# Kernel optimization log

Hardware: AMD Instinct MI355X
Metric: run time of the kernel (lower is better)

Reference implementation:

```python
import jax, jax.numpy as jnp
import numpy as np

D_MODEL = 1024
N_HEADS = 16
D_HEAD = D_MODEL // N_HEADS
SEQ_LEN = 4096
BATCH = 1
WINDOW = 256
NUM_RAND = 32
GLOBAL_TOKENS = (0,)


def _bigbird_mask(seq_len: int) -> jnp.ndarray:
    """Additive mask (0 = attend, -inf = blocked): global + sliding window + random.
    Random token selection is deterministic (fixed seed), mirroring torch.manual_seed(42)."""
    rng = np.random.default_rng(42)
    mask = np.full((seq_len, seq_len), -np.inf, dtype=np.float32)
    idx = np.arange(seq_len)
    # sliding window: |i-j| <= WINDOW (end = i + window + 1 in the original)
    band = np.abs(idx[:, None] - idx[None, :]) <= WINDOW
    mask[band] = 0.0
    # global tokens: full row + full column
    for g in GLOBAL_TOKENS:
        mask[g, :] = 0.0
        mask[:, g] = 0.0
    not_global = ~np.isin(idx, np.array(GLOBAL_TOKENS))
    gset = set(GLOBAL_TOKENS)
    for i in range(seq_len):
        if i in gset:
            continue
        cand = idx[(np.abs(idx - i) > WINDOW) & not_global]
        if cand.size >= NUM_RAND:
            sel = rng.choice(cand, size=NUM_RAND, replace=False)
            mask[i, sel] = 0.0
    return jnp.asarray(mask)


def setup_inputs() -> dict:
    key = jax.random.key(0)
    ks = jax.random.split(key, 9)
    s = 1.0 / np.sqrt(D_MODEL)
    x = jax.random.normal(ks[0], (BATCH, SEQ_LEN, D_MODEL), dtype=jnp.float32)
    # torch.nn.Linear weights are [out_features, in_features]
    Wq = jax.random.normal(ks[1], (D_MODEL, D_MODEL), dtype=jnp.float32) * s
    Wk = jax.random.normal(ks[2], (D_MODEL, D_MODEL), dtype=jnp.float32) * s
    Wv = jax.random.normal(ks[3], (D_MODEL, D_MODEL), dtype=jnp.float32) * s
    Wo = jax.random.normal(ks[4], (D_MODEL, D_MODEL), dtype=jnp.float32) * s
    bq = jax.random.normal(ks[5], (D_MODEL,), dtype=jnp.float32) * s
    bk = jax.random.normal(ks[6], (D_MODEL,), dtype=jnp.float32) * s
    bv = jax.random.normal(ks[7], (D_MODEL,), dtype=jnp.float32) * s
    bo = jax.random.normal(ks[8], (D_MODEL,), dtype=jnp.float32) * s
    mask = _bigbird_mask(SEQ_LEN)
    return {"x": x, "Wq": Wq, "bq": bq, "Wk": Wk, "bk": bk,
            "Wv": Wv, "bv": bv, "Wo": Wo, "bo": bo, "mask": mask}


def reference(x, Wq, bq, Wk, bk, Wv, bv, Wo, bo, mask):
    B, S, D = x.shape
    H, dh = N_HEADS, D_HEAD
    scale = dh ** -0.5
    q = (x @ Wq.T + bq).reshape(B, S, H, dh)  # [B,S,H,dh]
    k = (x @ Wk.T + bk).reshape(B, S, H, dh)
    v = (x @ Wv.T + bv).reshape(B, S, H, dh)
    scores = jnp.einsum("bihd,bjhd->bhij", q, k) * scale + mask  # [B,H,S,S]
    attn = jax.nn.softmax(scores, axis=-1)  # dropout is identity in eval mode
    out = jnp.einsum("bhij,bjhd->bihd", attn, v).reshape(B, S, D)
    return out @ Wo.T + bo
```

## Files before the change

kernel.cpp:

```cpp
#include <hip/hip_runtime.h>

typedef __attribute__((ext_vector_type(8))) short short8;
typedef __attribute__((ext_vector_type(4))) short short4v;
typedef __attribute__((ext_vector_type(4))) float f32x4;
typedef __attribute__((ext_vector_type(4))) float float4v;
typedef __attribute__((ext_vector_type(4))) unsigned uint4v;

#define MFMA16(a, b, c) __builtin_amdgcn_mfma_f32_16x16x32_bf16(a, b, c, 0, 0, 0)

static __device__ __forceinline__ short f2bf(float f) {
  union { float f; unsigned u; } a; a.f = f;
  unsigned r = a.u + 0x7fffu + ((a.u >> 16) & 1u);
  return (short)(r >> 16);
}
static __device__ __forceinline__ float bf2f(short s) {
  union { float f; unsigned u; } a; a.u = ((unsigned)(unsigned short)s) << 16;
  return a.f;
}
static __device__ __forceinline__ float u2f(unsigned u) {
  union { float f; unsigned u; } a; a.u = u;
  return a.f;
}

__global__ __launch_bounds__(256) void k_bitmask(const float* __restrict__ mask,
                                                 unsigned long long* __restrict__ bmT) {
  int wid = blockIdx.x * 4 + (threadIdx.x >> 6);
  int lane = threadIdx.x & 63;
  int ct = wid & 63, r = wid >> 6;
  float v = mask[(size_t)r * 4096 + ct * 64 + lane];
  unsigned long long bal = __ballot(v == 0.0f);
  if (lane == 0) bmT[(size_t)ct * 4096 + r] = bal;
}

__global__ __launch_bounds__(256) void k_randidx(const unsigned long long* __restrict__ bmT,
                                                 unsigned short* __restrict__ ridx,
                                                 unsigned* __restrict__ cntR) {
  int r = blockIdx.x * 4 + (threadIdx.x >> 6);
  int lane = threadIdx.x & 63;
  if (r == 0) {
    if (lane < 32) ridx[lane] = 0;
    if (lane == 0) cntR[0] = 0;
    return;
  }
  int rb = r >> 6;
  bool excl = (lane == 0) || (lane >= rb - 4 && lane <= rb + 4);
  unsigned long long w64 = excl ? 0ull : bmT[(size_t)lane * 4096 + r];
  int cnt = __popcll(w64);
  int p = cnt;
#pragma unroll
  for (int off = 1; off < 64; off <<= 1) {
    int t = __shfl_up(p, off);
    if (lane >= off) p += t;
  }
  int base = p - cnt;
  int total = __shfl(p, 63);
  while (w64) {
    int b = __ffsll((unsigned long long)w64) - 1;
    ridx[(size_t)r * 32 + base] = (unsigned short)(lane * 64 + b);
    ++base;
    w64 &= w64 - 1;
  }
  for (int t = total + lane; t < 32; t += 64) ridx[(size_t)r * 32 + t] = 0;
  if (lane == 63) cntR[r] = (unsigned)p;
}

__global__ __launch_bounds__(256) void k_split(const float* __restrict__ src,
                                               short* __restrict__ hi,
                                               short* __restrict__ lo, int n4) {
  int i = blockIdx.x * 256 + threadIdx.x;
  if (i >= n4) return;
  float4v x = ((const float4v*)src)[i];
  short4v h, l;
#pragma unroll
  for (int j = 0; j < 4; ++j) {
    short hh = f2bf(x[j]);
    h[j] = hh;
    l[j] = f2bf(x[j] - bf2f(hh));
  }
  ((short4v*)hi)[i] = h;
  ((short4v*)lo)[i] = l;
}

__global__ __launch_bounds__(256) void k_splitw(const float* __restrict__ wq,
                                                const float* __restrict__ wk,
                                                const float* __restrict__ wv,
                                                const float* __restrict__ wo,
                                                short* __restrict__ hi,
                                                short* __restrict__ lo) {
  int i = blockIdx.x * 256 + threadIdx.x;
  int row = i >> 8, c4 = i & 255;
  const float* src = row < 1024 ? wq + row * 1024
                   : row < 2048 ? wk + (row - 1024) * 1024
                   : row < 3072 ? wv + (row - 2048) * 1024
                                : wo + (row - 3072) * 1024;
  float4v x = ((const float4v*)src)[c4];
  short4v h, l;
#pragma unroll
  for (int j = 0; j < 4; ++j) {
    short hh = f2bf(x[j]);
    h[j] = hh;
    l[j] = f2bf(x[j] - bf2f(hh));
  }
  ((short4v*)hi)[i] = h;
  ((short4v*)lo)[i] = l;
}

template <int SPLIT, int EPI>
__global__ __launch_bounds__(256) void k_gemm(const short* __restrict__ Agh,
                                              const short* __restrict__ Agl,
                                              const short* __restrict__ Bgh,
                                              const short* __restrict__ Bgl,
                                              const float* __restrict__ b0,
                                              const float* __restrict__ b1,
                                              const float* __restrict__ b2,
                                              short* __restrict__ outb,
                                              float* __restrict__ outf) {
  const int K = 1024;
  const int LDT = 72;
  __shared__ short Ah[128 * LDT];
  __shared__ short Bh[128 * LDT];
  __shared__ short Al[SPLIT ? 128 * LDT : 8];
  __shared__ short Bl[SPLIT ? 128 * LDT : 8];
  int tid = threadIdx.x, lane = tid & 63, w = tid >> 6;
  int bm = blockIdx.x * 128, bn = blockIdx.y * 128;
  int wm = (w >> 1) * 64, wn = (w & 1) * 64;
  int arow = lane & 15, ag = lane >> 4;
  int srow = tid >> 3, sc = (tid & 7) * 8;
  f32x4 acc[4][4] = {};

  for (int k0 = 0; k0 < K; k0 += 64) {
    __syncthreads();
#pragma unroll
    for (int p = 0; p < 4; ++p) {
      int r = srow + p * 32;
      *(short8*)&Ah[r * LDT + sc] = *(const short8*)&Agh[(bm + r) * K + k0 + sc];
      *(short8*)&Bh[r * LDT + sc] = *(const short8*)&Bgh[(bn + r) * K + k0 + sc];
      if (SPLIT) {
        *(short8*)&Al[r * LDT + sc] = *(const short8*)&Agl[(bm + r) * K + k0 + sc];
        *(short8*)&Bl[r * LDT + sc] = *(const short8*)&Bgl[(bn + r) * K + k0 + sc];
      }
    }
    __syncthreads();
#pragma unroll
    for (int kk = 0; kk < 64; kk += 32) {
      int ko = kk + ag * 8;
      short8 af[4], bf[4], afl[4], bfl[4];
#pragma unroll
      for (int mi = 0; mi < 4; ++mi)
        af[mi] = *(const short8*)&Ah[(wm + mi * 16 + arow) * LDT + ko];
#pragma unroll
      for (int ni = 0; ni < 4; ++ni)
        bf[ni] = *(const short8*)&Bh[(wn + ni * 16 + arow) * LDT + ko];
      if (SPLIT) {
#pragma unroll
        for (int mi = 0; mi < 4; ++mi)
          afl[mi] = *(const short8*)&Al[(wm + mi * 16 + arow) * LDT + ko];
#pragma unroll
        for (int ni = 0; ni < 4; ++ni)
          bfl[ni] = *(const short8*)&Bl[(wn + ni * 16 + arow) * LDT + ko];
      }
#pragma unroll
      for (int mi = 0; mi < 4; ++mi)
#pragma unroll
        for (int ni = 0; ni < 4; ++ni) {
          acc[mi][ni] = MFMA16(af[mi], bf[ni], acc[mi][ni]);
          if (SPLIT) {
            acc[mi][ni] = MFMA16(af[mi], bfl[ni], acc[mi][ni]);
            acc[mi][ni] = MFMA16(afl[mi], bf[ni], acc[mi][ni]);
          }
        }
    }
  }
#pragma unroll
  for (int mi = 0; mi < 4; ++mi)
#pragma unroll
    for (int ni = 0; ni < 4; ++ni)
#pragma unroll
      for (int r = 0; r < 4; ++r) {
        int row = bm + wm + mi * 16 + ag * 4 + r;
        int col = bn + wn + ni * 16 + arow;
        float v = acc[mi][ni][r];
        if (EPI == 0) {
          int cl = col & 1023;
          const float* bp = col < 1024 ? b0 : col < 2048 ? b1 : b2;
          v += bp[cl];
          int head = cl >> 6, dh = col & 63, pr = col >> 10;
          outb[pr * (16 * 4096 * 64) + (head * 4096 + row) * 64 + dh] = f2bf(v);
        } else {
          v += b0[col];
          outf[row * 1024 + col] = v;
        }
      }
}

#define QS2 0.18033688f

__global__ __launch_bounds__(256) void k_rand(const short* __restrict__ q,
                                              const short* __restrict__ k,
                                              const short* __restrict__ v,
                                              const unsigned short* __restrict__ ridx,
                                              const unsigned* __restrict__ cntR,
                                              float* __restrict__ RO,
                                              float* __restrict__ RL) {
  __shared__ float Pp[4][4][32];
  __shared__ unsigned Pc[4][4][32];
  __shared__ float R0o[4][64];
  __shared__ float R0l[4];
  int tid = threadIdx.x, lane = tid & 63, w = tid >> 6;
  int bid = blockIdx.x;

  if (bid < 4096) {
    int head = bid & 15, rg = bid >> 4;
    int rbase = rg * 16 + w * 4;
    int rw = lane >> 4;
    int cl = lane & 15;
    int row = rbase + rw;
    const short* kh = k + (size_t)head * 4096 * 64;
    const short* vh = v + (size_t)head * 4096 * 64;
    unsigned cnt = cntR[row];
    unsigned col0 = ridx[(size_t)row * 32 + cl];
    unsigned col1 = ridx[(size_t)row * 32 + 16 + cl];
    const uint4v* qp4 = (const uint4v*)(q + ((size_t)head * 4096 + row) * 64);
    const uint4v* k0 = (const uint4v*)(kh + (size_t)col0 * 64);
    const uint4v* k1 = (const uint4v*)(kh + (size_t)col1 * 64);
    float s0 = 0.f, s1 = 0.f;
#pragma unroll
    for (int i = 0; i < 8; ++i) {
      uint4v qv = qp4[i];
      uint4v a = k0[i];
      uint4v b = k1[i];
#pragma unroll
      for (int jj = 0; jj < 4; ++jj) {
        float qlo = u2f(qv[jj] << 16), qhi = u2f(qv[jj] & 0xffff0000u);
        s0 = fmaf(qlo, u2f(a[jj] << 16), s0);
        s0 = fmaf(qhi, u2f(a[jj] & 0xffff0000u), s0);
        s1 = fmaf(qlo, u2f(b[jj] << 16), s1);
        s1 = fmaf(qhi, u2f(b[jj] & 0xffff0000u), s1);
      }
    }
    float p0 = (cl < (int)cnt) ? exp2f(fmaf(s0, QS2, -32.f)) : 0.f;
    float p1 = (cl + 16 < (int)cnt) ? exp2f(fmaf(s1, QS2, -32.f)) : 0.f;
    float ls = p0 + p1;
#pragma unroll
    for (int off = 1; off < 16; off <<= 1) ls += __shfl_xor(ls, off, 16);
    Pp[w][rw][cl] = p0;
    Pp[w][rw][16 + cl] = p1;
    Pc[w][rw][cl] = col0;
    Pc[w][rw][16 + cl] = col1;
    if (cl == 0 && row != 0) RL[(size_t)head * 4096 + row] = ls;
    int h2 = lane >> 5, r2 = (lane >> 3) & 3, ch = lane & 7;
    float o[8] = {};
#pragma unroll
    for (int i = 0; i < 16; ++i) {
      int ci = h2 * 16 + i;
      float pp = Pp[w][r2][ci];
      unsigned cc = Pc[w][r2][ci];
      uint4v vv = *(const uint4v*)(vh + (size_t)cc * 64 + ch * 8);
#pragma unroll
      for (int jj = 0; jj < 4; ++jj) {
        o[2 * jj] = fmaf(pp, u2f(vv[jj] << 16), o[2 * jj]);
        o[2 * jj + 1] = fmaf(pp, u2f(vv[jj] & 0xffff0000u), o[2 * jj + 1]);
      }
    }
#pragma unroll
    for (int jj = 0; jj < 8; ++jj) o[jj] += __shfl_xor(o[jj], 32);
    int row2 = rbase + r2;
    if (h2 == 0 && row2 != 0) {
      float4v a = {o[0], o[1], o[2], o[3]};
      float4v b = {o[4], o[5], o[6], o[7]};
      float* ro = RO + ((size_t)head * 4096 + row2) * 64 + ch * 8;
      *(float4v*)ro = a;
      *(float4v*)(ro + 4) = b;
    }
  } else {
    int head = bid - 4096;
    const short* kh = k + (size_t)head * 4096 * 64;
    const short* vh = v + (size_t)head * 4096 * 64;
    const uint4v* qp4 = (const uint4v*)(q + (size_t)head * 4096 * 64);
    uint4v qv[8];
#pragma unroll
    for (int i = 0; i < 8; ++i) qv[i] = qp4[i];
    float o[8] = {};
    float lacc = 0.f;
    int grp = lane >> 3, ch8 = lane & 7;
    float* Pw = (float*)Pp[w];
    for (int chk = w; chk < 59; chk += 4) {
      int cb = 320 + chk * 64;
      const uint4v* kp4 = (const uint4v*)(kh + (size_t)(cb + lane) * 64);
      float s2 = 0.f;
#pragma unroll
      for (int i = 0; i < 8; ++i) {
        uint4v kv = kp4[i];
#pragma unroll
        for (int jj = 0; jj < 4; ++jj) {
          s2 = fmaf(u2f(qv[i][jj] << 16), u2f(kv[jj] << 16), s2);
          s2 = fmaf(u2f(qv[i][jj] & 0xffff0000u), u2f(kv[jj] & 0xffff0000u), s2);
        }
      }
      float p = exp2f(fmaf(s2, QS2, -32.f));
      lacc += p;
      Pw[lane] = p;
#pragma unroll
      for (int i = 0; i < 8; ++i) {
        float pp = Pw[grp * 8 + i];
        uint4v vv = *(const uint4v*)(vh + (size_t)(cb + grp * 8 + i) * 64 + ch8 * 8);
#pragma unroll
        for (int jj = 0; jj < 4; ++jj) {
          o[2 * jj] = fmaf(pp, u2f(vv[jj] << 16), o[2 * jj]);
          o[2 * jj + 1] = fmaf(pp, u2f(vv[jj] & 0xffff0000u), o[2 * jj + 1]);
        }
      }
    }
#pragma unroll
    for (int off = 8; off < 64; off <<= 1) {
#pragma unroll
      for (int jj = 0; jj < 8; ++jj) o[jj] += __shfl_xor(o[jj], off);
      lacc += __shfl_xor(lacc, off);
    }
    lacc += __shfl_xor(lacc, 1);
    lacc += __shfl_xor(lacc, 2);
    lacc += __shfl_xor(lacc, 4);
    if (grp == 0) {
#pragma unroll
      for (int jj = 0; jj < 8; ++jj) R0o[w][ch8 * 8 + jj] = o[jj];
    }
    if (lane == 0) R0l[w] = lacc;
    __syncthreads();
    if (w == 0) {
      float o4 = R0o[0][lane] + R0o[1][lane] + R0o[2][lane] + R0o[3][lane];
      RO[(size_t)head * 4096 * 64 + lane] = o4;
      if (lane == 0) RL[(size_t)head * 4096] = R0l[0] + R0l[1] + R0l[2] + R0l[3];
    }
  }
}

__global__ __launch_bounds__(256) void k_flash(const short* __restrict__ q,
                                               const short* __restrict__ k,
                                               const short* __restrict__ v,
                                               const unsigned long long* __restrict__ bmT,
                                               const float* __restrict__ RO,
                                               const float* __restrict__ RL,
                                               short* __restrict__ aoh,
                                               short* __restrict__ aol) {
  const int LDT = 88;
  const int LDP = 72;
  __shared__ short Kl[64 * LDT];
  __shared__ short VT[64 * LDT];
  __shared__ short Pl[4 * 16 * LDP];
  __shared__ unsigned long long BM[64];
  int tid = threadIdx.x, lane = tid & 63, w = tid >> 6;
  int head = blockIdx.x & 15, rb = blockIdx.x >> 4;
  int q0 = rb * 64;
  int arow = lane & 15, ag = lane >> 4;
  int srow = tid >> 3, sc = (tid & 7) * 8;

  const short* qh = q + ((size_t)head * 4096 + q0 + w * 16) * 64;
  const short* kh = k + (size_t)head * 4096 * 64;
  const short* vh = v + (size_t)head * 4096 * 64;
  short8 aq0 = *(const short8*)&qh[arow * 64 + ag * 8];
  short8 aq1 = *(const short8*)&qh[arow * 64 + 32 + ag * 8];

  f32x4 accO[4] = {};
  float m[4] = {-1e30f, -1e30f, -1e30f, -1e30f};
  float lsum[4] = {0.f, 0.f, 0.f, 0.f};

  int t_lo = rb - 4; if (t_lo < 0) t_lo = 0;
  int t_hi = rb + 4; if (t_hi > 63) t_hi = 63;
  int extra0 = (t_lo > 0) ? 1 : 0;
  int nt = t_hi - t_lo + 1 + extra0;

  for (int it = 0; it < nt; ++it) {
    int ct = (extra0 && it == 0) ? 0 : t_lo + it - extra0;
    __syncthreads();
#pragma unroll
    for (int p = 0; p < 2; ++p) {
      int r = srow + p * 32;
      *(short8*)&Kl[r * LDT + sc] = *(const short8*)&kh[(ct * 64 + r) * 64 + sc];
    }
#pragma unroll
    for (int p = 0; p < 2; ++p) {
      int r = srow + p * 32;
      short8 vv = *(const short8*)&vh[(ct * 64 + r) * 64 + sc];
#pragma unroll
      for (int i = 0; i < 8; ++i) {
        int row = sc + i;
        VT[row * LDT + (r ^ (((row >> 3) & 7) << 3))] = vv[i];
      }
    }
    if (tid < 128)
      ((unsigned*)BM)[tid] = ((const unsigned*)(bmT + (size_t)ct * 4096 + q0))[tid];
    __syncthreads();

    f32x4 s[4];
    __builtin_amdgcn_s_setprio(1);
#pragma unroll
    for (int ni = 0; ni < 4; ++ni) {
      short8 b0 = *(const short8*)&Kl[(ni * 16 + arow) * LDT + ag * 8];
      short8 b1 = *(const short8*)&Kl[(ni * 16 + arow) * LDT + 32 + ag * 8];
      f32x4 z = {};
      z = MFMA16(aq0, b0, z);
      z = MFMA16(aq1, b1, z);
      s[ni] = z;
    }
    __builtin_amdgcn_s_setprio(0);
    float pv[4][4], mx[4];
#pragma unroll
    for (int r = 0; r < 4; ++r) {
      unsigned long long wrd = BM[w * 16 + ag * 4 + r];
      unsigned wlo = (unsigned)wrd, whi = (unsigned)(wrd >> 32);
      float rm = -1e30f;
#pragma unroll
      for (int ni = 0; ni < 4; ++ni) {
        unsigned word = (ni < 2) ? wlo : whi;
        unsigned bit = (word >> (arow + (ni & 1) * 16)) & 1u;
        float sv = s[ni][r] * QS2;
        sv = bit ? sv : -1e30f;
        pv[ni][r] = sv;
        rm = fmaxf(rm, sv);
      }
      mx[r] = rm;
    }
#pragma unroll
    for (int off = 1; off < 16; off <<= 1)
#pragma unroll
      for (int r = 0; r < 4; ++r) mx[r] = fmaxf(mx[r], __shfl_xor(mx[r], off, 16));
#pragma unroll
    for (int r = 0; r < 4; ++r) {
      float mnew = fmaxf(m[r], mx[r]);
      float alpha = exp2f(m[r] - mnew);
      m[r] = mnew;
      lsum[r] *= alpha;
      accO[0][r] *= alpha; accO[1][r] *= alpha;
      accO[2][r] *= alpha; accO[3][r] *= alpha;
      float rs = 0.f;
#pragma unroll
      for (int ni = 0; ni < 4; ++ni) {
        float p = exp2f(pv[ni][r] - mnew);
        pv[ni][r] = p;
        rs += p;
      }
#pragma unroll
      for (int off = 1; off < 16; off <<= 1) rs += __shfl_xor(rs, off, 16);
      lsum[r] += rs;
    }
    short* Pw = &Pl[w * 16 * LDP];
#pragma unroll
    for (int r = 0; r < 4; ++r)
#pragma unroll
      for (int ni = 0; ni < 4; ++ni)
        Pw[(ag * 4 + r) * LDP + ni * 16 + arow] = f2bf(pv[ni][r]);
    __builtin_amdgcn_s_setprio(1);
#pragma unroll
    for (int kk2 = 0; kk2 < 2; ++kk2) {
      short8 pa = *(const short8*)&Pw[arow * LDP + kk2 * 32 + ag * 8];
#pragma unroll
      for (int f = 0; f < 4; ++f) {
        int drow = f * 16 + arow;
        int jo = (kk2 * 32 + ag * 8) ^ (((drow >> 3) & 7) << 3);
        short8 vb = *(const short8*)&VT[drow * LDT + jo];
        accO[f] = MFMA16(pa, vb, accO[f]);
      }
    }
    __builtin_amdgcn_s_setprio(0);
  }

#pragma unroll
  for (int r = 0; r < 4; ++r) {
    int rr = ag * 4 + r;
    int row = q0 + w * 16 + rr;
    float mF = fmaxf(m[r], 32.0f);
    float ab = exp2f(m[r] - mF);
    float aR = exp2f(32.0f - mF);
    float lR = RL[(size_t)head * 4096 + row];
    float lt = lsum[r] * ab + lR * aR;
#pragma unroll
    for (int f = 0; f < 4; ++f) {
      float o = accO[f][r] * ab + RO[((size_t)head * 4096 + row) * 64 + f * 16 + arow] * aR;
      o /= lt;
      short hh = f2bf(o);
      size_t off = (size_t)row * 1024 + head * 64 + f * 16 + arow;
      aoh[off] = hh;
      aol[off] = f2bf(o - bf2f(hh));
    }
  }
}

extern "C" void kernel_launch(void* const* d_in, const int* in_sizes, int n_in,
                              void* d_out, int out_size, void* d_ws, size_t ws_size,
                              hipStream_t stream) {
  const float* x = (const float*)d_in[0];
  const float* Wq = (const float*)d_in[1];
  const float* bq = (const float*)d_in[2];
  const float* Wk = (const float*)d_in[3];
  const float* bk = (const float*)d_in[4];
  const float* Wv = (const float*)d_in[5];
  const float* bv = (const float*)d_in[6];
  const float* Wo = (const float*)d_in[7];
  const float* bo = (const float*)d_in[8];
  const float* mask = (const float*)d_in[9];

  char* ws = (char*)d_ws;
  unsigned long long* bmT = (unsigned long long*)(ws + 0);
  short* xh  = (short*)(ws + 2097152);
  short* xl  = (short*)(ws + 10485760);
  short* wh  = (short*)(ws + 18874368);
  short* wl  = (short*)(ws + 27262976);
  short* qkv = (short*)(ws + 35651584);
  unsigned short* ridx = (unsigned short*)(ws + 60817408);
  unsigned* cntR = (unsigned*)(ws + 61079552);
  float* RO = (float*)(ws + 61095936);
  float* RL = (float*)(ws + 77873152);
  short* aoh = xh;
  short* aol = xl;
  const int QSZ = 16 * 4096 * 64;
  float* outf = (float*)d_out;

  k_bitmask<<<dim3(65536), dim3(256), 0, stream>>>(mask, bmT);
  k_randidx<<<dim3(1024), dim3(256), 0, stream>>>(bmT, ridx, cntR);
  k_split<<<dim3(4096), dim3(256), 0, stream>>>(x, xh, xl, 1048576);
  k_splitw<<<dim3(4096), dim3(256), 0, stream>>>(Wq, Wk, Wv, Wo, wh, wl);
  k_gemm<1, 0><<<dim3(32, 24), dim3(256), 0, stream>>>(
      xh, xl, wh, wl, bq, bk, bv, qkv, nullptr);
  k_rand<<<dim3(4112), dim3(256), 0, stream>>>(qkv, qkv + QSZ, qkv + 2 * QSZ,
                                               ridx, cntR, RO, RL);
  k_flash<<<dim3(1024), dim3(256), 0, stream>>>(qkv, qkv + QSZ, qkv + 2 * QSZ, bmT,
                                                RO, RL, aoh, aol);
  k_gemm<1, 1><<<dim3(32, 8), dim3(256), 0, stream>>>(
      aoh, aol, wh + 3072 * 1024, wl + 3072 * 1024, bo, nullptr, nullptr, nullptr, outf);
}
```

Before: 408.8 us.

## Replace split-bf16 three-pass GEMMs with single-pass fp16 MFMA throughout

Drops the hi/lo bf16 split emulation of fp32 in both projection GEMMs, using a single fp16 operand and one MFMA per tile instead of three. Q/K/V, the attention probabilities and the attention output are stored as fp16, and the scalar random-attention paths decode fp16. The intent is to cut MFMA work, shared-memory traffic and conversion bandwidth to roughly a third. The cost is lower accuracy, since fp16 has a narrow range and 10-bit mantissa, which could exceed tolerance or overflow.

```diff
diff --git a/kernel.cpp b/kernel.cpp
--- a/kernel.cpp
+++ b/kernel.cpp
@@ -1,25 +1,23 @@
 #include <hip/hip_runtime.h>
 
 typedef __attribute__((ext_vector_type(8))) short short8;
-typedef __attribute__((ext_vector_type(4))) short short4v;
+typedef __attribute__((ext_vector_type(8))) _Float16 half8;
 typedef __attribute__((ext_vector_type(4))) float f32x4;
 typedef __attribute__((ext_vector_type(4))) float float4v;
 typedef __attribute__((ext_vector_type(4))) unsigned uint4v;
 
-#define MFMA16(a, b, c) __builtin_amdgcn_mfma_f32_16x16x32_bf16(a, b, c, 0, 0, 0)
-
-static __device__ __forceinline__ short f2bf(float f) {
-  union { float f; unsigned u; } a; a.f = f;
-  unsigned r = a.u + 0x7fffu + ((a.u >> 16) & 1u);
-  return (short)(r >> 16);
-}
-static __device__ __forceinline__ float bf2f(short s) {
-  union { float f; unsigned u; } a; a.u = ((unsigned)(unsigned short)s) << 16;
-  return a.f;
-}
-static __device__ __forceinline__ float u2f(unsigned u) {
-  union { float f; unsigned u; } a; a.u = u;
-  return a.f;
+#define MFMA16(a, b, c) __builtin_amdgcn_mfma_f32_16x16x32_f16(a, b, c, 0, 0, 0)
+
+static __device__ __forceinline__ short f2h(float f) {
+  _Float16 h = (_Float16)f;
+  short s;
+  __builtin_memcpy(&s, &h, 2);
+  return s;
+}
+static __device__ __forceinline__ float h2f(unsigned short u) {
+  _Float16 h;
+  __builtin_memcpy(&h, &u, 2);
+  return (float)h;
 }
 
 __global__ __launch_bounds__(256) void k_bitmask(const float* __restrict__ mask,
@@ -64,52 +62,46 @@
   if (lane == 63) cntR[r] = (unsigned)p;
 }
 
-__global__ __launch_bounds__(256) void k_split(const float* __restrict__ src,
-                                               short* __restrict__ hi,
-                                               short* __restrict__ lo, int n4) {
+__global__ __launch_bounds__(256) void k_cvt(const float* __restrict__ src,
+                                             short* __restrict__ dst, int n8) {
   int i = blockIdx.x * 256 + threadIdx.x;
-  if (i >= n4) return;
-  float4v x = ((const float4v*)src)[i];
-  short4v h, l;
+  if (i >= n8) return;
+  float4v a = ((const float4v*)src)[2 * i];
+  float4v b = ((const float4v*)src)[2 * i + 1];
+  short8 o;
 #pragma unroll
   for (int j = 0; j < 4; ++j) {
-    short hh = f2bf(x[j]);
-    h[j] = hh;
-    l[j] = f2bf(x[j] - bf2f(hh));
-  }
-  ((short4v*)hi)[i] = h;
-  ((short4v*)lo)[i] = l;
-}
-
-__global__ __launch_bounds__(256) void k_splitw(const float* __restrict__ wq,
-                                                const float* __restrict__ wk,
-                                                const float* __restrict__ wv,
-                                                const float* __restrict__ wo,
-                                                short* __restrict__ hi,
-                                                short* __restrict__ lo) {
+    o[j] = f2h(a[j]);
+    o[4 + j] = f2h(b[j]);
+  }
+  ((short8*)dst)[i] = o;
+}
+
+__global__ __launch_bounds__(256) void k_cvtw(const float* __restrict__ wq,
+                                              const float* __restrict__ wk,
+                                              const float* __restrict__ wv,
+                                              const float* __restrict__ wo,
+                                              short* __restrict__ dst) {
   int i = blockIdx.x * 256 + threadIdx.x;
-  int row = i >> 8, c4 = i & 255;
+  int row = i >> 7, c8 = i & 127;
   const float* src = row < 1024 ? wq + row * 1024
                    : row < 2048 ? wk + (row - 1024) * 1024
                    : row < 3072 ? wv + (row - 2048) * 1024
                                 : wo + (row - 3072) * 1024;
-  float4v x = ((const float4v*)src)[c4];
-  short4v h, l;
+  float4v a = ((const float4v*)src)[2 * c8];
+  float4v b = ((const float4v*)src)[2 * c8 + 1];
+  short8 o;
 #pragma unroll
   for (int j = 0; j < 4; ++j) {
-    short hh = f2bf(x[j]);
-    h[j] = hh;
-    l[j] = f2bf(x[j] - bf2f(hh));
-  }
-  ((short4v*)hi)[i] = h;
-  ((short4v*)lo)[i] = l;
-}
-
-template <int SPLIT, int EPI>
-__global__ __launch_bounds__(256) void k_gemm(const short* __restrict__ Agh,
-                                              const short* __restrict__ Agl,
-                                              const short* __restrict__ Bgh,
-                                              const short* __restrict__ Bgl,
+    o[j] = f2h(a[j]);
+    o[4 + j] = f2h(b[j]);
+  }
+  ((short8*)dst)[i] = o;
+}
+
+template <int EPI>
+__global__ __launch_bounds__(256) void k_gemm(const short* __restrict__ Ag,
+                                              const short* __restrict__ Bg,
                                               const float* __restrict__ b0,
                                               const float* __restrict__ b1,
                                               const float* __restrict__ b2,
@@ -119,8 +111,6 @@
   const int LDT = 72;
   __shared__ short Ah[128 * LDT];
   __shared__ short Bh[128 * LDT];
-  __shared__ short Al[SPLIT ? 128 * LDT : 8];
-  __shared__ short Bl[SPLIT ? 128 * LDT : 8];
   int tid = threadIdx.x, lane = tid & 63, w = tid >> 6;
   int bm = blockIdx.x * 128, bn = blockIdx.y * 128;
   int wm = (w >> 1) * 64, wn = (w & 1) * 64;
@@ -133,42 +123,25 @@
 #pragma unroll
     for (int p = 0; p < 4; ++p) {
       int r = srow + p * 32;
-      *(short8*)&Ah[r * LDT + sc] = *(const short8*)&Agh[(bm + r) * K + k0 + sc];
-      *(short8*)&Bh[r * LDT + sc] = *(const short8*)&Bgh[(bn + r) * K + k0 + sc];
-      if (SPLIT) {
-        *(short8*)&Al[r * LDT + sc] = *(const short8*)&Agl[(bm + r) * K + k0 + sc];
-        *(short8*)&Bl[r * LDT + sc] = *(const short8*)&Bgl[(bn + r) * K + k0 + sc];
-      }
+      *(short8*)&Ah[r * LDT + sc] = *(const short8*)&Ag[(bm + r) * K + k0 + sc];
+      *(short8*)&Bh[r * LDT + sc] = *(const short8*)&Bg[(bn + r) * K + k0 + sc];
     }
     __syncthreads();
 #pragma unroll
     for (int kk = 0; kk < 64; kk += 32) {
       int ko = kk + ag * 8;
-      short8 af[4], bf[4], afl[4], bfl[4];
+      half8 af[4], bf[4];
 #pragma unroll
       for (int mi = 0; mi < 4; ++mi)
-        af[mi] = *(const short8*)&Ah[(wm + mi * 16 + arow) * LDT + ko];
+        af[mi] = *(const half8*)&Ah[(wm + mi * 16 + arow) * LDT + ko];
 #pragma unroll
       for (int ni = 0; ni < 4; ++ni)
-        bf[ni] = *(const short8*)&Bh[(wn + ni * 16 + arow) * LDT + ko];
-      if (SPLIT) {
-#pragma unroll
-        for (int mi = 0; mi < 4; ++mi)
-          afl[mi] = *(const short8*)&Al[(wm + mi * 16 + arow) * LDT + ko];
+        bf[ni] = *(const half8*)&Bh[(wn + ni * 16 + arow) * LDT + ko];
+#pragma unroll
+      for (int mi = 0; mi < 4; ++mi)
 #pragma unroll
         for (int ni = 0; ni < 4; ++ni)
-          bfl[ni] = *(const short8*)&Bl[(wn + ni * 16 + arow) * LDT + ko];
-      }
-#pragma unroll
-      for (int mi = 0; mi < 4; ++mi)
-#pragma unroll
-        for (int ni = 0; ni < 4; ++ni) {
           acc[mi][ni] = MFMA16(af[mi], bf[ni], acc[mi][ni]);
-          if (SPLIT) {
-            acc[mi][ni] = MFMA16(af[mi], bfl[ni], acc[mi][ni]);
-            acc[mi][ni] = MFMA16(afl[mi], bf[ni], acc[mi][ni]);
-          }
-        }
     }
   }
 #pragma unroll
@@ -185,7 +158,7 @@
           const float* bp = col < 1024 ? b0 : col < 2048 ? b1 : b2;
           v += bp[cl];
           int head = cl >> 6, dh = col & 63, pr = col >> 10;
-          outb[pr * (16 * 4096 * 64) + (head * 4096 + row) * 64 + dh] = f2bf(v);
+          outb[pr * (16 * 4096 * 64) + (head * 4096 + row) * 64 + dh] = f2h(v);
         } else {
           v += b0[col];
           outf[row * 1024 + col] = v;
@@ -231,11 +204,12 @@
       uint4v b = k1[i];
 #pragma unroll
       for (int jj = 0; jj < 4; ++jj) {
-        float qlo = u2f(qv[jj] << 16), qhi = u2f(qv[jj] & 0xffff0000u);
-        s0 = fmaf(qlo, u2f(a[jj] << 16), s0);
-        s0 = fmaf(qhi, u2f(a[jj] & 0xffff0000u), s0);
-        s1 = fmaf(qlo, u2f(b[jj] << 16), s1);
-        s1 = fmaf(qhi, u2f(b[jj] & 0xffff0000u), s1);
+        float qlo = h2f((unsigned short)(qv[jj] & 0xffffu));
+        float qhi = h2f((unsigned short)(qv[jj] >> 16));
+        s0 = fmaf(qlo, h2f((unsigned short)(a[jj] & 0xffffu)), s0);
+        s0 = fmaf(qhi, h2f((unsigned short)(a[jj] >> 16)), s0);
+        s1 = fmaf(qlo, h2f((unsigned short)(b[jj] & 0xffffu)), s1);
+        s1 = fmaf(qhi, h2f((unsigned short)(b[jj] >> 16)), s1);
       }
     }
     float p0 = (cl < (int)cnt) ? exp2f(fmaf(s0, QS2, -32.f)) : 0.f;
@@ -258,8 +232,8 @@
       uint4v vv = *(const uint4v*)(vh + (size_t)cc * 64 + ch * 8);
 #pragma unroll
       for (int jj = 0; jj < 4; ++jj) {
-        o[2 * jj] = fmaf(pp, u2f(vv[jj] << 16), o[2 * jj]);
-        o[2 * jj + 1] = fmaf(pp, u2f(vv[jj] & 0xffff0000u), o[2 * jj + 1]);
+        o[2 * jj] = fmaf(pp, h2f((unsigned short)(vv[jj] & 0xffffu)), o[2 * jj]);
+        o[2 * jj + 1] = fmaf(pp, h2f((unsigned short)(vv[jj] >> 16)), o[2 * jj + 1]);
       }
     }
 #pragma unroll
@@ -293,8 +267,10 @@
         uint4v kv = kp4[i];
 #pragma unroll
         for (int jj = 0; jj < 4; ++jj) {
-          s2 = fmaf(u2f(qv[i][jj] << 16), u2f(kv[jj] << 16), s2);
-          s2 = fmaf(u2f(qv[i][jj] & 0xffff0000u), u2f(kv[jj] & 0xffff0000u), s2);
+          s2 = fmaf(h2f((unsigned short)(qv[i][jj] & 0xffffu)),
+                    h2f((unsigned short)(kv[jj] & 0xffffu)), s2);
+          s2 = fmaf(h2f((unsigned short)(qv[i][jj] >> 16)),
+                    h2f((unsigned short)(kv[jj] >> 16)), s2);
         }
       }
       float p = exp2f(fmaf(s2, QS2, -32.f));
@@ -306,8 +282,8 @@
         uint4v vv = *(const uint4v*)(vh + (size_t)(cb + grp * 8 + i) * 64 + ch8 * 8);
 #pragma unroll
         for (int jj = 0; jj < 4; ++jj) {
-          o[2 * jj] = fmaf(pp, u2f(vv[jj] << 16), o[2 * jj]);
-          o[2 * jj + 1] = fmaf(pp, u2f(vv[jj] & 0xffff0000u), o[2 * jj + 1]);
+          o[2 * jj] = fmaf(pp, h2f((unsigned short)(vv[jj] & 0xffffu)), o[2 * jj]);
+          o[2 * jj + 1] = fmaf(pp, h2f((unsigned short)(vv[jj] >> 16)), o[2 * jj + 1]);
         }
       }
     }
@@ -340,8 +316,7 @@
                                                const unsigned long long* __restrict__ bmT,
                                                const float* __restrict__ RO,
                                                const float* __restrict__ RL,
-                                               short* __restrict__ aoh,
-                                               short* __restrict__ aol) {
+                                               short* __restrict__ ao) {
   const int LDT = 88;
   const int LDP = 72;
   __shared__ short Kl[64 * LDT];
@@ -357,8 +332,8 @@
   const short* qh = q + ((size_t)head * 4096 + q0 + w * 16) * 64;
   const short* kh = k + (size_t)head * 4096 * 64;
   const short* vh = v + (size_t)head * 4096 * 64;
-  short8 aq0 = *(const short8*)&qh[arow * 64 + ag * 8];
-  short8 aq1 = *(const short8*)&qh[arow * 64 + 32 + ag * 8];
+  half8 aq0 = *(const half8*)&qh[arow * 64 + ag * 8];
+  half8 aq1 = *(const half8*)&qh[arow * 64 + 32 + ag * 8];
 
   f32x4 accO[4] = {};
   float m[4] = {-1e30f, -1e30f, -1e30f, -1e30f};
@@ -395,8 +370,8 @@
     __builtin_amdgcn_s_setprio(1);
 #pragma unroll
     for (int ni = 0; ni < 4; ++ni) {
-      short8 b0 = *(const short8*)&Kl[(ni * 16 + arow) * LDT + ag * 8];
-      short8 b1 = *(const short8*)&Kl[(ni * 16 + arow) * LDT + 32 + ag * 8];
+      half8 b0 = *(const half8*)&Kl[(ni * 16 + arow) * LDT + ag * 8];
+      half8 b1 = *(const half8*)&Kl[(ni * 16 + arow) * LDT + 32 + ag * 8];
       f32x4 z = {};
       z = MFMA16(aq0, b0, z);
       z = MFMA16(aq1, b1, z);
@@ -448,16 +423,16 @@
     for (int r = 0; r < 4; ++r)
 #pragma unroll
       for (int ni = 0; ni < 4; ++ni)
-        Pw[(ag * 4 + r) * LDP + ni * 16 + arow] = f2bf(pv[ni][r]);
+        Pw[(ag * 4 + r) * LDP + ni * 16 + arow] = f2h(pv[ni][r]);
     __builtin_amdgcn_s_setprio(1);
 #pragma unroll
     for (int kk2 = 0; kk2 < 2; ++kk2) {
-      short8 pa = *(const short8*)&Pw[arow * LDP + kk2 * 32 + ag * 8];
+      half8 pa = *(const half8*)&Pw[arow * LDP + kk2 * 32 + ag * 8];
 #pragma unroll
       for (int f = 0; f < 4; ++f) {
         int drow = f * 16 + arow;
         int jo = (kk2 * 32 + ag * 8) ^ (((drow >> 3) & 7) << 3);
-        short8 vb = *(const short8*)&VT[drow * LDT + jo];
+        half8 vb = *(const half8*)&VT[drow * LDT + jo];
         accO[f] = MFMA16(pa, vb, accO[f]);
       }
     }
@@ -477,10 +452,7 @@
     for (int f = 0; f < 4; ++f) {
       float o = accO[f][r] * ab + RO[((size_t)head * 4096 + row) * 64 + f * 16 + arow] * aR;
       o /= lt;
-      short hh = f2bf(o);
-      size_t off = (size_t)row * 1024 + head * 64 + f * 16 + arow;
-      aoh[off] = hh;
-      aol[off] = f2bf(o - bf2f(hh));
+      ao[(size_t)row * 1024 + head * 64 + f * 16 + arow] = f2h(o);
     }
   }
 }
@@ -502,29 +474,26 @@
   char* ws = (char*)d_ws;
   unsigned long long* bmT = (unsigned long long*)(ws + 0);
   short* xh  = (short*)(ws + 2097152);
-  short* xl  = (short*)(ws + 10485760);
-  short* wh  = (short*)(ws + 18874368);
-  short* wl  = (short*)(ws + 27262976);
-  short* qkv = (short*)(ws + 35651584);
-  unsigned short* ridx = (unsigned short*)(ws + 60817408);
-  unsigned* cntR = (unsigned*)(ws + 61079552);
-  float* RO = (float*)(ws + 61095936);
-  float* RL = (float*)(ws + 77873152);
-  short* aoh = xh;
-  short* aol = xl;
+  short* wh  = (short*)(ws + 10485760);
+  short* qkv = (short*)(ws + 18874368);
+  unsigned short* ridx = (unsigned short*)(ws + 44040192);
+  unsigned* cntR = (unsigned*)(ws + 44302336);
+  float* RO = (float*)(ws + 44318720);
+  float* RL = (float*)(ws + 61095936);
+  short* ao = xh;
   const int QSZ = 16 * 4096 * 64;
   float* outf = (float*)d_out;
 
   k_bitmask<<<dim3(65536), dim3(256), 0, stream>>>(mask, bmT);
   k_randidx<<<dim3(1024), dim3(256), 0, stream>>>(bmT, ridx, cntR);
-  k_split<<<dim3(4096), dim3(256), 0, stream>>>(x, xh, xl, 1048576);
-  k_splitw<<<dim3(4096), dim3(256), 0, stream>>>(Wq, Wk, Wv, Wo, wh, wl);
-  k_gemm<1, 0><<<dim3(32, 24), dim3(256), 0, stream>>>(
-      xh, xl, wh, wl, bq, bk, bv, qkv, nullptr);
+  k_cvt<<<dim3(2048), dim3(256), 0, stream>>>(x, xh, 524288);
+  k_cvtw<<<dim3(2048), dim3(256), 0, stream>>>(Wq, Wk, Wv, Wo, wh);
+  k_gemm<0><<<dim3(32, 24), dim3(256), 0, stream>>>(
+      xh, wh, bq, bk, bv, qkv, nullptr);
   k_rand<<<dim3(4112), dim3(256), 0, stream>>>(qkv, qkv + QSZ, qkv + 2 * QSZ,
                                                ridx, cntR, RO, RL);
   k_flash<<<dim3(1024), dim3(256), 0, stream>>>(qkv, qkv + QSZ, qkv + 2 * QSZ, bmT,
-                                                RO, RL, aoh, aol);
-  k_gemm<1, 1><<<dim3(32, 8), dim3(256), 0, stream>>>(
-      aoh, aol, wh + 3072 * 1024, wl + 3072 * 1024, bo, nullptr, nullptr, nullptr, outf);
-}
+                                                RO, RL, ao);
+  k_gemm<1><<<dim3(32, 8), dim3(256), 0, stream>>>(
+      ao, wh + 3072 * 1024, bo, nullptr, nullptr, nullptr, outf);
+}
```

Measured after the change: 336.1 us. 17.8% less time.
